# Performance work log

Measured on AMD Instinct MI355X. Metric: run time of the kernel, lower is better.

The kernel has to match this reference:

```python
import jax, jax.numpy as jnp
import numpy as np

N_NODES = 50000
N_EDGES = 800000
F_EXP = 128
F_CNV = 64
HID = 128
N_CLASSES = 10
N_GRAPHS = 64
SLOPE = 0.2


def setup_inputs() -> dict:
    key = jax.random.key(0)
    ks = jax.random.split(key, 24)
    inp = {
        "exp": jax.random.normal(ks[0], (N_NODES, F_EXP), dtype=jnp.float32),
        "cnv": jax.random.normal(ks[1], (N_NODES, F_CNV), dtype=jnp.float32),
        "edge_index": jax.random.randint(ks[2], (2, N_EDGES), 0, N_NODES, dtype=jnp.int64 if jax.config.jax_enable_x64 else jnp.int32),
        "batch": jnp.sort(jax.random.randint(ks[3], (N_NODES,), 0, N_GRAPHS)),
    }
    s = 0.02
    def lin(k, fi, fo):
        kw, kb = jax.random.split(k)
        return (jax.random.normal(kw, (fi, fo), jnp.float32) * s,
                jax.random.normal(kb, (fo,), jnp.float32) * s)
    inp["eps1e"] = jnp.zeros((), jnp.float32)
    inp["W1e"], inp["b1e"] = lin(ks[4], F_EXP, HID)
    inp["eps2e"] = jnp.zeros((), jnp.float32)
    inp["W2e"], inp["b2e"] = lin(ks[5], HID, HID)
    inp["eps1c"] = jnp.zeros((), jnp.float32)
    inp["W1c"], inp["b1c"] = lin(ks[6], F_CNV, HID)
    inp["eps2c"] = jnp.zeros((), jnp.float32)
    inp["W2c"], inp["b2c"] = lin(ks[7], HID, HID)
    inp["Wm"], inp["bm"] = lin(ks[8], 2 * HID, HID)
    inp["Wp1"], inp["bp1"] = lin(ks[9], HID, HID)
    inp["Wp2"], inp["bp2"] = lin(ks[10], HID, N_CLASSES)
    return inp


def _lrelu(x):
    return jnp.where(x > 0, x, SLOPE * x)


def _forward(exp, cnv, src, dst, batch,
             eps1e, W1e, b1e, eps2e, W2e, b2e,
             eps1c, W1c, b1c, eps2c, W2c, b2c,
             Wm, bm, Wp1, bp1, Wp2, bp2):
    N = exp.shape[0]

    def gin(x, eps, W, b):
        # scatter-add neighbor aggregation over edges (self-loops included in src/dst)
        agg = jax.ops.segment_sum(x[src], dst, num_segments=N)
        return ((1.0 + eps) * x + agg) @ W + b

    x_exp = _lrelu(gin(exp, eps1e, W1e, b1e))
    x_exp = _lrelu(gin(x_exp, eps2e, W2e, b2e))
    x_cnv = _lrelu(gin(cnv, eps1c, W1c, b1c))
    x_cnv = _lrelu(gin(x_cnv, eps2c, W2c, b2c))
    x = jnp.concatenate([x_exp, x_cnv], axis=1) @ Wm + bm
    x = _lrelu(x)

    # global mean pool over graph ids
    counts = jax.ops.segment_sum(jnp.ones((N,), x.dtype), batch, num_segments=N_GRAPHS)
    counts = jnp.maximum(counts, 1.0)[:, None]
    graph_repr = jax.ops.segment_sum(x, batch, num_segments=N_GRAPHS) / counts

    logits_nodes = _lrelu(x @ Wp1 + bp1)  # nn.ReLU in mlp -> actually ReLU
    logits_nodes = jnp.maximum(x @ Wp1 + bp1, 0.0) @ Wp2 + bp2
    graph_logits = jax.ops.segment_sum(logits_nodes, batch, num_segments=N_GRAPHS) / counts
    return graph_repr, graph_logits


def reference(exp, cnv, edge_index, batch,
              eps1e, W1e, b1e, eps2e, W2e, b2e,
              eps1c, W1c, b1c, eps2c, W2c, b2c,
              Wm, bm, Wp1, bp1, Wp2, bp2):
    N = exp.shape[0]
    loop = jnp.arange(N, dtype=edge_index.dtype)
    src = jnp.concatenate([edge_index[0], loop])
    dst = jnp.concatenate([edge_index[1], loop])
    return _forward(exp, cnv, src, dst, batch,
                    eps1e, W1e, b1e, eps2e, W2e, b2e,
                    eps1c, W1c, b1c, eps2c, W2c, b2c,
                    Wm, bm, Wp1, bp1, Wp2, bp2)
```

## Files before the change

kernel.cpp:

```cpp
#include <hip/hip_runtime.h>

#define N_NODES 50000
#define N_PAD   50016
#define N_EDGES 800000
#define HID 128
#define NCLS 10
#define NG 64
#define PWAVE 32
#define NB_SCAN ((N_NODES + 255) / 256)

#define EPART 8
#define PRANGE ((N_NODES + EPART - 1) / EPART)
#define ECHUNK 4096
#define NCHUNK ((N_EDGES + ECHUNK - 1) / ECHUNK)

typedef unsigned int uint32;
typedef __attribute__((ext_vector_type(8))) short bf16x8;
typedef __attribute__((ext_vector_type(4))) float f32x4;

__device__ __forceinline__ unsigned short f2bf(float f) {
    uint32 u = __float_as_uint(f);
    uint32 r = u + 0x7fffu + ((u >> 16) & 1u);
    return (unsigned short)(r >> 16);
}
__device__ __forceinline__ float bflo(uint32 v) { return __uint_as_float(v << 16); }
__device__ __forceinline__ float bfhi(uint32 v) { return __uint_as_float(v & 0xffff0000u); }
__device__ __forceinline__ uint32 packbf(float a, float b) {
    return (uint32)f2bf(a) | ((uint32)f2bf(b) << 16);
}


#define PRE_N4E (N_NODES * 128 / 4)
#define PRE_N4C (N_NODES * 64 / 4)
#define PRE_CB ((PRE_N4E + PRE_N4C + 255) / 256)
#define PRE_ZB ((N_NODES + 255) / 256)
#define PRE_TOTAL (PRE_CB + PRE_ZB + 1 + PRE_ZB + 416)

__global__ __launch_bounds__(256) void pre_k(const float* __restrict__ exp_f,
                                             unsigned short* __restrict__ Xe,
                                             const float* __restrict__ cnv_f,
                                             unsigned short* __restrict__ Xc,
                                             int* __restrict__ deg,
                                             float* __restrict__ sums,
                                             const int* __restrict__ batch,
                                             int* __restrict__ gstart,
                                             const float* W1e, const float* W2e,
                                             const float* W1c, const float* W2c,
                                             const float* Wm, const float* Wp1,
                                             unsigned short* WT1e, unsigned short* WT2e,
                                             unsigned short* WT1c, unsigned short* WT2c,
                                             unsigned short* WTm1, unsigned short* WTm2,
                                             unsigned short* WTp1) {
    int b = blockIdx.x;
    int t = threadIdx.x;
    if (b < PRE_CB) {
        int i = b * 256 + t;
        const float* in;
        unsigned short* out;
        if (i < PRE_N4E) { in = exp_f; out = Xe; }
        else { i -= PRE_N4E; if (i >= PRE_N4C) return; in = cnv_f; out = Xc; }
        float4 v = *(const float4*)(in + (size_t)i * 4);
        uint2 o = {packbf(v.x, v.y), packbf(v.z, v.w)};
        *(uint2*)(out + (size_t)i * 4) = o;
        return;
    }
    b -= PRE_CB;
    if (b < PRE_ZB) {
        int i = b * 256 + t;
        if (i < N_NODES) deg[i] = 0;
        return;
    }
    b -= PRE_ZB;
    if (b == 0) {
        for (int i = t; i < 2 * NG * 128; i += 256) sums[i] = 0.f;
        return;
    }
    b -= 1;
    if (b < PRE_ZB) {
        int i = b * 256 + t;
        if (i >= N_NODES) return;
        int bb = batch[i];
        int prev = (i == 0) ? -1 : batch[i - 1];
        for (int g = prev + 1; g <= bb; g++) gstart[g] = i;
        if (i == N_NODES - 1) {
            for (int g = bb + 1; g <= NG; g++) gstart[g] = N_NODES;
        }
        return;
    }
    b -= PRE_ZB;
    const float* W; unsigned short* WT; int i; int K;
    if (b < 64)       { W = W1e; WT = WT1e; i = b * 256 + t;          K = 128; }
    else if (b < 128) { W = W2e; WT = WT2e; i = (b - 64) * 256 + t;   K = 128; }
    else if (b < 160) { W = W1c; WT = WT1c; i = (b - 128) * 256 + t;  K = 64;  }
    else if (b < 224) { W = W2c; WT = WT2c; i = (b - 160) * 256 + t;  K = 128; }
    else if (b < 352) {
        i = (b - 224) * 256 + t;
        int k = i >> 7, n = i & 127;
        unsigned short v = f2bf(Wm[i]);
        if (k < 128) WTm1[n * 128 + k] = v;
        else         WTm2[n * 128 + (k - 128)] = v;
        return;
    }
    else              { W = Wp1; WT = WTp1; i = (b - 352) * 256 + t;  K = 128; }
    int k = i >> 7, n = i & 127;
    if (k < K) WT[n * K + k] = f2bf(W[i]);
}


__global__ __launch_bounds__(256) void count_part_k(const int* __restrict__ dst,
                                                    int* __restrict__ deg) {
    int part = blockIdx.x & 7;
    int chunk = blockIdx.x >> 3;
    int lo = part * PRANGE;
    int hi = min(lo + PRANGE, N_NODES);
    int e0 = chunk * ECHUNK;
    int e1 = min(e0 + ECHUNK, N_EDGES);
    for (int i = e0 + threadIdx.x; i < e1; i += 256) {
        int d = dst[i];
        if (d >= lo && d < hi) atomicAdd(&deg[d], 1);
    }
}

__global__ __launch_bounds__(256) void scatter_part_k(const int* __restrict__ src,
                                                      const int* __restrict__ dst,
                                                      int* __restrict__ cursor,
                                                      int* __restrict__ csr) {
    int part = blockIdx.x & 7;
    int chunk = blockIdx.x >> 3;
    int lo = part * PRANGE;
    int hi = min(lo + PRANGE, N_NODES);
    int e0 = chunk * ECHUNK;
    int e1 = min(e0 + ECHUNK, N_EDGES);
    for (int i = e0 + threadIdx.x; i < e1; i += 256) {
        int d = dst[i];
        if (d >= lo && d < hi) {
            int pos = atomicAdd(&cursor[d], 1);
            csr[pos] = src[i];
        }
    }
}

__device__ __forceinline__ int block_excl_scan_256(int v, int tid, int* total_out) {
    int lane = tid & 63, w = tid >> 6;
    int x = v;
#pragma unroll
    for (int off = 1; off < 64; off <<= 1) {
        int y = __shfl_up(x, off, 64);
        if (lane >= off) x += y;
    }
    __shared__ int wsum[4];
    if (lane == 63) wsum[w] = x;
    __syncthreads();
    int add = 0;
#pragma unroll
    for (int i = 0; i < 4; i++) add += (i < w) ? wsum[i] : 0;
    int total = wsum[0] + wsum[1] + wsum[2] + wsum[3];
    if (total_out) *total_out = total;
    return x - v + add;
}

__global__ __launch_bounds__(256) void scan_partial_k(const int* __restrict__ deg,
                                                      int* __restrict__ rowptr,
                                                      int* __restrict__ blocksum) {
    int tid = threadIdx.x;
    int gid = blockIdx.x * 256 + tid;
    int v = (gid < N_NODES) ? deg[gid] : 0;
    int total;
    int excl = block_excl_scan_256(v, tid, &total);
    if (gid < N_NODES) rowptr[gid] = excl;
    if (tid == 0) blocksum[blockIdx.x] = total;
}

__global__ __launch_bounds__(256) void scan_root_k(const int* __restrict__ blocksum,
                                                   int* __restrict__ blockoff,
                                                   const int* __restrict__ gstart,
                                                   float* __restrict__ invcnt) {
    int tid = threadIdx.x;
    int v = (tid < NB_SCAN) ? blocksum[tid] : 0;
    int excl = block_excl_scan_256(v, tid, nullptr);
    if (tid < NB_SCAN) blockoff[tid] = excl;
    if (tid < NG) {
        int c = gstart[tid + 1] - gstart[tid];
        invcnt[tid] = (c > 0) ? 1.0f / (float)c : 0.0f;
    }
}

__global__ __launch_bounds__(256) void scan_add_k(int* __restrict__ rowptr,
                                                  int* __restrict__ cursor,
                                                  const int* __restrict__ blockoff) {
    int gid = blockIdx.x * 256 + threadIdx.x;
    if (gid < N_NODES) {
        int r = rowptr[gid] + blockoff[blockIdx.x];
        rowptr[gid] = r;
        cursor[gid] = r;
    }
    if (gid == 0) rowptr[N_NODES] = N_EDGES;
}


__device__ __forceinline__ uint32 agg_row128(const uint32* __restrict__ X,
                                             const int* __restrict__ rowptr,
                                             const int* __restrict__ csr,
                                             int n, int lane, float scale) {
    uint32 xv = X[(size_t)n * 64 + lane];
    float a0 = scale * bflo(xv);
    float a1 = scale * bfhi(xv);
    int e = rowptr[n], e1 = rowptr[n + 1];
    for (; e + 16 <= e1; e += 16) {
        int idx[16]; uint32 vv[16];
#pragma unroll
        for (int j = 0; j < 16; j++) idx[j] = csr[e + j];
#pragma unroll
        for (int j = 0; j < 16; j++) vv[j] = X[(size_t)idx[j] * 64 + lane];
#pragma unroll
        for (int j = 0; j < 16; j++) { a0 += bflo(vv[j]); a1 += bfhi(vv[j]); }
    }
    if (e + 8 <= e1) {
        int idx[8]; uint32 vv[8];
#pragma unroll
        for (int j = 0; j < 8; j++) idx[j] = csr[e + j];
#pragma unroll
        for (int j = 0; j < 8; j++) vv[j] = X[(size_t)idx[j] * 64 + lane];
#pragma unroll
        for (int j = 0; j < 8; j++) { a0 += bflo(vv[j]); a1 += bfhi(vv[j]); }
        e += 8;
    }
    if (e + 4 <= e1) {
        int idx[4]; uint32 vv[4];
#pragma unroll
        for (int j = 0; j < 4; j++) idx[j] = csr[e + j];
#pragma unroll
        for (int j = 0; j < 4; j++) vv[j] = X[(size_t)idx[j] * 64 + lane];
#pragma unroll
        for (int j = 0; j < 4; j++) { a0 += bflo(vv[j]); a1 += bfhi(vv[j]); }
        e += 4;
    }
    for (; e < e1; e++) {
        uint32 v = X[(size_t)csr[e] * 64 + lane];
        a0 += bflo(v);
        a1 += bfhi(v);
    }
    return packbf(a0, a1);
}

__device__ __forceinline__ uint32 agg_row64(const uint32* __restrict__ X,
                                            const int* __restrict__ rowptr,
                                            const int* __restrict__ csr,
                                            int n, int lane32, float scale) {
    uint32 xv = X[(size_t)n * 32 + lane32];
    float a0 = scale * bflo(xv);
    float a1 = scale * bfhi(xv);
    int e = rowptr[n], e1 = rowptr[n + 1];
    for (; e + 8 <= e1; e += 8) {
        int idx[8]; uint32 vv[8];
#pragma unroll
        for (int j = 0; j < 8; j++) idx[j] = csr[e + j];
#pragma unroll
        for (int j = 0; j < 8; j++) vv[j] = X[(size_t)idx[j] * 32 + lane32];
#pragma unroll
        for (int j = 0; j < 8; j++) { a0 += bflo(vv[j]); a1 += bfhi(vv[j]); }
    }
    if (e + 4 <= e1) {
        int idx[4]; uint32 vv[4];
#pragma unroll
        for (int j = 0; j < 4; j++) idx[j] = csr[e + j];
#pragma unroll
        for (int j = 0; j < 4; j++) vv[j] = X[(size_t)idx[j] * 32 + lane32];
#pragma unroll
        for (int j = 0; j < 4; j++) { a0 += bflo(vv[j]); a1 += bfhi(vv[j]); }
        e += 4;
    }
    for (; e < e1; e++) {
        uint32 v = X[(size_t)csr[e] * 32 + lane32];
        a0 += bflo(v);
        a1 += bfhi(v);
    }
    return packbf(a0, a1);
}


__global__ __launch_bounds__(256) void agg_gemm_k(const uint32* __restrict__ X1,
                                                  const float* __restrict__ eps1,
                                                  const unsigned short* __restrict__ WT1p,
                                                  const float* __restrict__ b1,
                                                  unsigned short* __restrict__ out1,
                                                  const uint32* __restrict__ X2,
                                                  const float* __restrict__ eps2,
                                                  const unsigned short* __restrict__ WT2p,
                                                  const float* __restrict__ b2,
                                                  unsigned short* __restrict__ out2,
                                                  const int* __restrict__ rowptr,
                                                  const int* __restrict__ csr,
                                                  int nblk1, int K2) {
    __shared__ uint32 lds[32 * 64];
    int blk = blockIdx.x;
    bool second = blk >= nblk1;
    if (second) blk -= nblk1;
    const uint32* X = second ? X2 : X1;
    const float* epsp = second ? eps2 : eps1;
    const unsigned short* WT = second ? WT2p : WT1p;
    const float* bias = second ? b2 : b1;
    unsigned short* out = second ? out2 : out1;
    int K = second ? K2 : 128;

    int tid = threadIdx.x;
    int w = tid >> 6, lane = tid & 63;
    int base = blk * 32;
    float scale = 2.0f + epsp[0];

    if (K == 128) {
        for (int s = 0; s < 8; s++) {
            int lrow = w * 8 + s;
            int n = base + lrow;
            uint32 outv = 0;
            if (n < N_NODES) outv = agg_row128(X, rowptr, csr, n, lane, scale);
            int byte = (lrow * 256 + lane * 4) ^ ((lrow & 7) << 4);
            lds[byte >> 2] = outv;
        }
    } else {
        int half = lane >> 5, lane32 = lane & 31;
        for (int s = 0; s < 4; s++) {
            int lrow = w * 8 + 2 * s + half;
            int n = base + lrow;
            uint32 outv = 0;
            if (n < N_NODES) outv = agg_row64(X, rowptr, csr, n, lane32, scale);
            int byte = (lrow * 128 + lane32 * 4) ^ ((lrow & 7) << 4);
            lds[byte >> 2] = outv;
        }
    }
    __syncthreads();

    int m = lane & 15, g = lane >> 4;
    int lrow = (w & 1) * 16 + m;
    int row16 = base + (w & 1) * 16;
    int col16 = (w >> 1) * 64;

    f32x4 acc[4];
#pragma unroll
    for (int nt = 0; nt < 4; nt++) acc[nt] = (f32x4){0.f, 0.f, 0.f, 0.f};

    const unsigned short* bp = WT + (size_t)(col16 + m) * K + g * 8;
    int rowbytes = K * 2;
    for (int k0 = 0; k0 < K; k0 += 32) {
        int ab = (lrow * rowbytes + (g * 8 + k0) * 2) ^ ((lrow & 7) << 4);
        bf16x8 af = *(const bf16x8*)((const char*)lds + ab);
#pragma unroll
        for (int nt = 0; nt < 4; nt++) {
            bf16x8 bfv = *(const bf16x8*)(bp + (size_t)nt * 16 * K + k0);
            acc[nt] = __builtin_amdgcn_mfma_f32_16x16x32_bf16(af, bfv, acc[nt], 0, 0, 0);
        }
    }

#pragma unroll
    for (int nt = 0; nt < 4; nt++) {
        int col = col16 + nt * 16 + m;
        float bv = bias[col];
#pragma unroll
        for (int r = 0; r < 4; r++) {
            int row = row16 + g * 4 + r;
            if (row < N_NODES) {
                float v = acc[nt][r] + bv;
                v = v > 0.f ? v : 0.2f * v;
                out[(size_t)row * 128 + col] = f2bf(v);
            }
        }
    }
}


__global__ __launch_bounds__(256) void gemm_bf_k(const unsigned short* __restrict__ A1,
                                                 const unsigned short* __restrict__ WT1, int K1,
                                                 const unsigned short* __restrict__ A2,
                                                 const unsigned short* __restrict__ WT2, int K2,
                                                 const float* __restrict__ bias,
                                                 unsigned short* __restrict__ out, int act) {
    int tid = threadIdx.x;
    int w = tid >> 6, l = tid & 63;
    int row16 = blockIdx.x * 32 + (w & 1) * 16;
    int col16 = (w >> 1) * 64;
    int m = l & 15, g = l >> 4;

    f32x4 acc[4];
#pragma unroll
    for (int nt = 0; nt < 4; nt++) acc[nt] = (f32x4){0.f, 0.f, 0.f, 0.f};

    const unsigned short* A = A1;
    const unsigned short* WT = WT1;
    int K = K1;
    for (int pass = 0; pass < 2; ++pass) {
        if (pass) {
            if (A2 == nullptr) break;
            A = A2; WT = WT2; K = K2;
        }
        const unsigned short* ap = A + (size_t)(row16 + m) * K + g * 8;
        const unsigned short* bp = WT + (size_t)(col16 + m) * K + g * 8;
        for (int k0 = 0; k0 < K; k0 += 32) {
            bf16x8 af = *(const bf16x8*)(ap + k0);
#pragma unroll
            for (int nt = 0; nt < 4; nt++) {
                bf16x8 bfv = *(const bf16x8*)(bp + (size_t)nt * 16 * K + k0);
                acc[nt] = __builtin_amdgcn_mfma_f32_16x16x32_bf16(af, bfv, acc[nt], 0, 0, 0);
            }
        }
    }

#pragma unroll
    for (int nt = 0; nt < 4; nt++) {
        int col = col16 + nt * 16 + m;
        float bv = bias[col];
#pragma unroll
        for (int r = 0; r < 4; r++) {
            int row = row16 + g * 4 + r;
            if (row < N_NODES) {
                float v = acc[nt][r] + bv;
                if (act == 1) v = v > 0.f ? v : 0.2f * v;
                else if (act == 2) v = fmaxf(v, 0.f);
                out[(size_t)row * 128 + col] = f2bf(v);
            }
        }
    }
}


__global__ __launch_bounds__(256) void pool2_bf_k(const uint32* __restrict__ D,
                                                  const uint32* __restrict__ T,
                                                  const int* __restrict__ batch,
                                                  float* __restrict__ sumD,
                                                  float* __restrict__ sumT) {
    int wv = (blockIdx.x * 256 + threadIdx.x) >> 6;
    int f = threadIdx.x & 63;
    int i0 = wv * PWAVE;
    if (i0 >= N_NODES) return;
    int i1 = min(i0 + PWAVE, N_NODES);
    float d0 = 0.f, d1 = 0.f, t0 = 0.f, t1 = 0.f;
    int g = batch[i0];
    int i = i0;
    for (; i + 4 <= i1; i += 4) {
        int b0 = batch[i], b1 = batch[i + 1], b2 = batch[i + 2], b3 = batch[i + 3];
        uint32 dv0 = D[(size_t)i * 64 + f];
        uint32 dv1 = D[(size_t)(i + 1) * 64 + f];
        uint32 dv2 = D[(size_t)(i + 2) * 64 + f];
        uint32 dv3 = D[(size_t)(i + 3) * 64 + f];
        uint32 tv0 = T[(size_t)i * 64 + f];
        uint32 tv1 = T[(size_t)(i + 1) * 64 + f];
        uint32 tv2 = T[(size_t)(i + 2) * 64 + f];
        uint32 tv3 = T[(size_t)(i + 3) * 64 + f];
#define POOL_STEP(bg, dv, tv)                                          \
        if (bg != g) {                                                 \
            atomicAdd(&sumD[g * 128 + 2 * f], d0);                     \
            atomicAdd(&sumD[g * 128 + 2 * f + 1], d1);                 \
            atomicAdd(&sumT[g * 128 + 2 * f], t0);                     \
            atomicAdd(&sumT[g * 128 + 2 * f + 1], t1);                 \
            d0 = d1 = t0 = t1 = 0.f; g = bg;                           \
        }                                                              \
        d0 += bflo(dv); d1 += bfhi(dv);                                \
        t0 += bflo(tv); t1 += bfhi(tv);
        POOL_STEP(b0, dv0, tv0)
        POOL_STEP(b1, dv1, tv1)
        POOL_STEP(b2, dv2, tv2)
        POOL_STEP(b3, dv3, tv3)
    }
    for (; i < i1; i++) {
        int bg = batch[i];
        uint32 dv = D[(size_t)i * 64 + f];
        uint32 tv = T[(size_t)i * 64 + f];
        POOL_STEP(bg, dv, tv)
    }
#undef POOL_STEP
    atomicAdd(&sumD[g * 128 + 2 * f], d0);
    atomicAdd(&sumD[g * 128 + 2 * f + 1], d1);
    atomicAdd(&sumT[g * 128 + 2 * f], t0);
    atomicAdd(&sumT[g * 128 + 2 * f + 1], t1);
}


__global__ __launch_bounds__(128) void finalize_k(const float* __restrict__ sumD,
                                                  const float* __restrict__ sumT,
                                                  const float* __restrict__ invcnt,
                                                  const float* __restrict__ Wp2,
                                                  const float* __restrict__ bp2,
                                                  float* __restrict__ out) {
    __shared__ float tr[128];
    int g = blockIdx.x;
    int f = threadIdx.x;
    float ic = invcnt[g];
    out[g * 128 + f] = sumD[g * 128 + f] * ic;
    tr[f] = sumT[g * 128 + f] * ic;
    __syncthreads();
    if (f < NCLS) {
        float acc = (ic > 0.f) ? bp2[f] : 0.f;
        for (int k = 0; k < 128; k++) acc = fmaf(tr[k], Wp2[k * NCLS + f], acc);
        out[NG * 128 + g * NCLS + f] = acc;
    }
}


extern "C" void kernel_launch(void* const* d_in, const int* in_sizes, int n_in,
                              void* d_out, int out_size, void* d_ws, size_t ws_size,
                              hipStream_t stream) {
    const float* exp_f = (const float*)d_in[0];
    const float* cnv_f = (const float*)d_in[1];
    const int*   ei    = (const int*)d_in[2];
    const int*   batch = (const int*)d_in[3];
    const float* eps1e = (const float*)d_in[4];
    const float* W1e   = (const float*)d_in[5];
    const float* b1e   = (const float*)d_in[6];
    const float* eps2e = (const float*)d_in[7];
    const float* W2e   = (const float*)d_in[8];
    const float* b2e   = (const float*)d_in[9];
    const float* eps1c = (const float*)d_in[10];
    const float* W1c   = (const float*)d_in[11];
    const float* b1c   = (const float*)d_in[12];
    const float* eps2c = (const float*)d_in[13];
    const float* W2c   = (const float*)d_in[14];
    const float* b2c   = (const float*)d_in[15];
    const float* Wm    = (const float*)d_in[16];
    const float* bm    = (const float*)d_in[17];
    const float* Wp1   = (const float*)d_in[18];
    const float* bp1   = (const float*)d_in[19];
    const float* Wp2   = (const float*)d_in[20];
    const float* bp2   = (const float*)d_in[21];
    float* out = (float*)d_out;

    char* ws = (char*)d_ws;
    size_t off = 0;
    auto alloc = [&](size_t bytes) -> void* {
        void* p = ws + off;
        off = (off + bytes + 255) & ~(size_t)255;
        return p;
    };
    int* deg      = (int*)alloc((size_t)N_NODES * 4);
    int* rowptr   = (int*)alloc((size_t)(N_NODES + 1) * 4);
    int* cursor   = (int*)alloc((size_t)N_NODES * 4);
    int* csr      = (int*)alloc((size_t)N_EDGES * 4);
    int* gstart   = (int*)alloc((NG + 1) * 4);
    float* invcnt = (float*)alloc(NG * 4);
    int* blocksum = (int*)alloc(NB_SCAN * 4);
    int* blockoff = (int*)alloc(NB_SCAN * 4);
    float* sumD   = (float*)alloc((size_t)NG * 128 * 4);
    float* sumT   = (float*)alloc((size_t)NG * 128 * 4);

    unsigned short* Xe = (unsigned short*)alloc((size_t)N_PAD * 128 * 2);
    unsigned short* Xc = (unsigned short*)alloc((size_t)N_PAD * 64 * 2);
    unsigned short* B  = (unsigned short*)alloc((size_t)N_PAD * 128 * 2);
    unsigned short* C  = (unsigned short*)alloc((size_t)N_PAD * 128 * 2);
    unsigned short* B2 = (unsigned short*)alloc((size_t)N_PAD * 128 * 2);
    unsigned short* C2 = (unsigned short*)alloc((size_t)N_PAD * 128 * 2);
    unsigned short* D  = (unsigned short*)alloc((size_t)N_PAD * 128 * 2);
    unsigned short* T  = (unsigned short*)alloc((size_t)N_PAD * 128 * 2);

    unsigned short* WT1e = (unsigned short*)alloc(128 * 128 * 2);
    unsigned short* WT2e = (unsigned short*)alloc(128 * 128 * 2);
    unsigned short* WT1c = (unsigned short*)alloc(128 * 64 * 2);
    unsigned short* WT2c = (unsigned short*)alloc(128 * 128 * 2);
    unsigned short* WTm1 = (unsigned short*)alloc(128 * 128 * 2);
    unsigned short* WTm2 = (unsigned short*)alloc(128 * 128 * 2);
    unsigned short* WTp1 = (unsigned short*)alloc(128 * 128 * 2);

    const int* src = ei;
    const int* dst = ei + N_EDGES;

    pre_k<<<PRE_TOTAL, 256, 0, stream>>>(exp_f, Xe, cnv_f, Xc, deg, sumD, batch, gstart,
                                         W1e, W2e, W1c, W2c, Wm, Wp1,
                                         WT1e, WT2e, WT1c, WT2c, WTm1, WTm2, WTp1);
    count_part_k<<<NCHUNK * EPART, 256, 0, stream>>>(dst, deg);
    scan_partial_k<<<NB_SCAN, 256, 0, stream>>>(deg, rowptr, blocksum);
    scan_root_k<<<1, 256, 0, stream>>>(blocksum, blockoff, gstart, invcnt);
    scan_add_k<<<NB_SCAN, 256, 0, stream>>>(rowptr, cursor, blockoff);
    scatter_part_k<<<NCHUNK * EPART, 256, 0, stream>>>(src, dst, cursor, csr);

    const int GEMM_GRID = (N_NODES + 31) / 32;

    agg_gemm_k<<<2 * GEMM_GRID, 256, 0, stream>>>((const uint32*)Xe, eps1e, WT1e, b1e, B,
                                                  (const uint32*)Xc, eps1c, WT1c, b1c, C,
                                                  rowptr, csr, GEMM_GRID, 64);
    agg_gemm_k<<<2 * GEMM_GRID, 256, 0, stream>>>((const uint32*)B, eps2e, WT2e, b2e, B2,
                                                  (const uint32*)C, eps2c, WT2c, b2c, C2,
                                                  rowptr, csr, GEMM_GRID, 128);
    gemm_bf_k<<<GEMM_GRID, 256, 0, stream>>>(B2, WTm1, 128, C2, WTm2, 128, bm, D, 1);
    gemm_bf_k<<<GEMM_GRID, 256, 0, stream>>>(D, WTp1, 128, nullptr, nullptr, 0, bp1, T, 2);
    const int POOL_GRID = ((N_NODES + PWAVE - 1) / PWAVE * 64 + 255) / 256;
    pool2_bf_k<<<POOL_GRID, 256, 0, stream>>>((const uint32*)D, (const uint32*)T,
                                              batch, sumD, sumT);
    finalize_k<<<NG, 128, 0, stream>>>(sumD, sumT, invcnt, Wp2, bp2, out);
}
```

Measured before the change: 458.0 us.

## Fuse mix GEMM, head GEMM and mean pooling into one LDS-staged kernel

Replaces the two gemm_bf_k launches and the pool kernel with a single kernel. It computes the mix layer tile, stages it in swizzled shared memory, runs the head GEMM from LDS, and pools both results per block with atomics. This drops the D and T global round trips and two launches, at the cost of more per-block atomics (32-row blocks instead of 32-row waves) and extra syncs. It also shrinks the aggregation inner unroll from 16 to 8 edges, which lowers register pressure but exposes fewer loads in flight.

```diff
diff --git a/kernel.cpp b/kernel.cpp
--- a/kernel.cpp
+++ b/kernel.cpp
@@ -6,7 +6,6 @@
 #define HID 128
 #define NCLS 10
 #define NG 64
-#define PWAVE 32
 #define NB_SCAN ((N_NODES + 255) / 256)
 
 #define EPART 8
@@ -206,16 +205,7 @@
     float a0 = scale * bflo(xv);
     float a1 = scale * bfhi(xv);
     int e = rowptr[n], e1 = rowptr[n + 1];
-    for (; e + 16 <= e1; e += 16) {
-        int idx[16]; uint32 vv[16];
-#pragma unroll
-        for (int j = 0; j < 16; j++) idx[j] = csr[e + j];
-#pragma unroll
-        for (int j = 0; j < 16; j++) vv[j] = X[(size_t)idx[j] * 64 + lane];
-#pragma unroll
-        for (int j = 0; j < 16; j++) { a0 += bflo(vv[j]); a1 += bfhi(vv[j]); }
-    }
-    if (e + 8 <= e1) {
+    for (; e + 8 <= e1; e += 8) {
         int idx[8]; uint32 vv[8];
 #pragma unroll
         for (int j = 0; j < 8; j++) idx[j] = csr[e + j];
@@ -223,7 +213,6 @@
         for (int j = 0; j < 8; j++) vv[j] = X[(size_t)idx[j] * 64 + lane];
 #pragma unroll
         for (int j = 0; j < 8; j++) { a0 += bflo(vv[j]); a1 += bfhi(vv[j]); }
-        e += 8;
     }
     if (e + 4 <= e1) {
         int idx[4]; uint32 vv[4];
@@ -368,109 +357,125 @@
 }
 
 
-__global__ __launch_bounds__(256) void gemm_bf_k(const unsigned short* __restrict__ A1,
-                                                 const unsigned short* __restrict__ WT1, int K1,
-                                                 const unsigned short* __restrict__ A2,
-                                                 const unsigned short* __restrict__ WT2, int K2,
-                                                 const float* __restrict__ bias,
-                                                 unsigned short* __restrict__ out, int act) {
+__global__ __launch_bounds__(256) void mix_head_pool_k(const unsigned short* __restrict__ B2,
+                                                       const unsigned short* __restrict__ WTm1,
+                                                       const unsigned short* __restrict__ C2,
+                                                       const unsigned short* __restrict__ WTm2,
+                                                       const float* __restrict__ bm,
+                                                       const unsigned short* __restrict__ WTp1,
+                                                       const float* __restrict__ bp1,
+                                                       const int* __restrict__ batch,
+                                                       float* __restrict__ sumD,
+                                                       float* __restrict__ sumT,
+                                                       float* __restrict__ outD) {
+    __shared__ uint32 Dl[32 * 64];
+    __shared__ uint32 Tl[32 * 64];
+    __shared__ int bat[32];
     int tid = threadIdx.x;
-    int w = tid >> 6, l = tid & 63;
-    int row16 = blockIdx.x * 32 + (w & 1) * 16;
+    int w = tid >> 6, lane = tid & 63;
+    int base = blockIdx.x * 32;
+    int m = lane & 15, g = lane >> 4;
+    int row16loc = (w & 1) * 16;
+    int row16 = base + row16loc;
     int col16 = (w >> 1) * 64;
-    int m = l & 15, g = l >> 4;
+
+    if (tid < 32) bat[tid] = (base + tid < N_NODES) ? batch[base + tid] : -1;
 
     f32x4 acc[4];
 #pragma unroll
     for (int nt = 0; nt < 4; nt++) acc[nt] = (f32x4){0.f, 0.f, 0.f, 0.f};
-
-    const unsigned short* A = A1;
-    const unsigned short* WT = WT1;
-    int K = K1;
     for (int pass = 0; pass < 2; ++pass) {
-        if (pass) {
-            if (A2 == nullptr) break;
-            A = A2; WT = WT2; K = K2;
-        }
-        const unsigned short* ap = A + (size_t)(row16 + m) * K + g * 8;
-        const unsigned short* bp = WT + (size_t)(col16 + m) * K + g * 8;
-        for (int k0 = 0; k0 < K; k0 += 32) {
+        const unsigned short* A = pass ? C2 : B2;
+        const unsigned short* WT = pass ? WTm2 : WTm1;
+        const unsigned short* ap = A + (size_t)(row16 + m) * 128 + g * 8;
+        const unsigned short* bp = WT + (size_t)(col16 + m) * 128 + g * 8;
+#pragma unroll
+        for (int k0 = 0; k0 < 128; k0 += 32) {
             bf16x8 af = *(const bf16x8*)(ap + k0);
 #pragma unroll
             for (int nt = 0; nt < 4; nt++) {
-                bf16x8 bfv = *(const bf16x8*)(bp + (size_t)nt * 16 * K + k0);
+                bf16x8 bfv = *(const bf16x8*)(bp + (size_t)nt * 16 * 128 + k0);
                 acc[nt] = __builtin_amdgcn_mfma_f32_16x16x32_bf16(af, bfv, acc[nt], 0, 0, 0);
             }
         }
     }
-
 #pragma unroll
     for (int nt = 0; nt < 4; nt++) {
         int col = col16 + nt * 16 + m;
-        float bv = bias[col];
+        float bv = bm[col];
 #pragma unroll
         for (int r = 0; r < 4; r++) {
-            int row = row16 + g * 4 + r;
-            if (row < N_NODES) {
-                float v = acc[nt][r] + bv;
-                if (act == 1) v = v > 0.f ? v : 0.2f * v;
-                else if (act == 2) v = fmaxf(v, 0.f);
-                out[(size_t)row * 128 + col] = f2bf(v);
+            int rl = row16loc + g * 4 + r;
+            float v = acc[nt][r] + bv;
+            v = v > 0.f ? v : 0.2f * v;
+            int byte = (rl * 256 + col * 2) ^ ((rl & 7) << 4);
+            *(unsigned short*)((char*)Dl + byte) = f2bf(v);
+        }
+    }
+    __syncthreads();
+
+    f32x4 acc2[4];
+#pragma unroll
+    for (int nt = 0; nt < 4; nt++) acc2[nt] = (f32x4){0.f, 0.f, 0.f, 0.f};
+    {
+        int lrowA = row16loc + m;
+        const unsigned short* bp = WTp1 + (size_t)(col16 + m) * 128 + g * 8;
+#pragma unroll
+        for (int k0 = 0; k0 < 128; k0 += 32) {
+            int ab = (lrowA * 256 + (g * 8 + k0) * 2) ^ ((lrowA & 7) << 4);
+            bf16x8 af = *(const bf16x8*)((const char*)Dl + ab);
+#pragma unroll
+            for (int nt = 0; nt < 4; nt++) {
+                bf16x8 bfv = *(const bf16x8*)(bp + (size_t)nt * 16 * 128 + k0);
+                acc2[nt] = __builtin_amdgcn_mfma_f32_16x16x32_bf16(af, bfv, acc2[nt], 0, 0, 0);
             }
         }
     }
-}
-
-
-__global__ __launch_bounds__(256) void pool2_bf_k(const uint32* __restrict__ D,
-                                                  const uint32* __restrict__ T,
-                                                  const int* __restrict__ batch,
-                                                  float* __restrict__ sumD,
-                                                  float* __restrict__ sumT) {
-    int wv = (blockIdx.x * 256 + threadIdx.x) >> 6;
-    int f = threadIdx.x & 63;
-    int i0 = wv * PWAVE;
-    if (i0 >= N_NODES) return;
-    int i1 = min(i0 + PWAVE, N_NODES);
-    float d0 = 0.f, d1 = 0.f, t0 = 0.f, t1 = 0.f;
-    int g = batch[i0];
-    int i = i0;
-    for (; i + 4 <= i1; i += 4) {
-        int b0 = batch[i], b1 = batch[i + 1], b2 = batch[i + 2], b3 = batch[i + 3];
-        uint32 dv0 = D[(size_t)i * 64 + f];
-        uint32 dv1 = D[(size_t)(i + 1) * 64 + f];
-        uint32 dv2 = D[(size_t)(i + 2) * 64 + f];
-        uint32 dv3 = D[(size_t)(i + 3) * 64 + f];
-        uint32 tv0 = T[(size_t)i * 64 + f];
-        uint32 tv1 = T[(size_t)(i + 1) * 64 + f];
-        uint32 tv2 = T[(size_t)(i + 2) * 64 + f];
-        uint32 tv3 = T[(size_t)(i + 3) * 64 + f];
-#define POOL_STEP(bg, dv, tv)                                          \
-        if (bg != g) {                                                 \
-            atomicAdd(&sumD[g * 128 + 2 * f], d0);                     \
-            atomicAdd(&sumD[g * 128 + 2 * f + 1], d1);                 \
-            atomicAdd(&sumT[g * 128 + 2 * f], t0);                     \
-            atomicAdd(&sumT[g * 128 + 2 * f + 1], t1);                 \
-            d0 = d1 = t0 = t1 = 0.f; g = bg;                           \
-        }                                                              \
-        d0 += bflo(dv); d1 += bfhi(dv);                                \
-        t0 += bflo(tv); t1 += bfhi(tv);
-        POOL_STEP(b0, dv0, tv0)
-        POOL_STEP(b1, dv1, tv1)
-        POOL_STEP(b2, dv2, tv2)
-        POOL_STEP(b3, dv3, tv3)
-    }
-    for (; i < i1; i++) {
-        int bg = batch[i];
-        uint32 dv = D[(size_t)i * 64 + f];
-        uint32 tv = T[(size_t)i * 64 + f];
-        POOL_STEP(bg, dv, tv)
-    }
-#undef POOL_STEP
-    atomicAdd(&sumD[g * 128 + 2 * f], d0);
-    atomicAdd(&sumD[g * 128 + 2 * f + 1], d1);
-    atomicAdd(&sumT[g * 128 + 2 * f], t0);
-    atomicAdd(&sumT[g * 128 + 2 * f + 1], t1);
+#pragma unroll
+    for (int nt = 0; nt < 4; nt++) {
+        int col = col16 + nt * 16 + m;
+        float bv = bp1[col];
+#pragma unroll
+        for (int r = 0; r < 4; r++) {
+            int rl = row16loc + g * 4 + r;
+            float v = fmaxf(acc2[nt][r] + bv, 0.f);
+            int byte = (rl * 256 + col * 2) ^ ((rl & 7) << 4);
+            *(unsigned short*)((char*)Tl + byte) = f2bf(v);
+        }
+    }
+    __syncthreads();
+
+    if (tid < 128) {
+        int cp = tid & 63;
+        int half = tid >> 6;
+        int r0 = half * 16;
+        int nrow = min(32, N_NODES - base);
+        int rend = min(r0 + 16, nrow);
+        if (r0 < rend) {
+            float d0 = 0.f, d1 = 0.f, t0 = 0.f, t1 = 0.f;
+            int gcur = bat[r0];
+            for (int r = r0; r < rend; r++) {
+                int bg = bat[r];
+                if (bg != gcur) {
+                    atomicAdd(&sumD[gcur * 128 + 2 * cp], d0);
+                    atomicAdd(&sumD[gcur * 128 + 2 * cp + 1], d1);
+                    atomicAdd(&sumT[gcur * 128 + 2 * cp], t0);
+                    atomicAdd(&sumT[gcur * 128 + 2 * cp + 1], t1);
+                    d0 = d1 = t0 = t1 = 0.f; gcur = bg;
+                }
+                int byte = (r * 256 + cp * 4) ^ ((r & 7) << 4);
+                uint32 dv = *(const uint32*)((const char*)Dl + byte);
+                uint32 tv = *(const uint32*)((const char*)Tl + byte);
+                d0 += bflo(dv); d1 += bfhi(dv);
+                t0 += bflo(tv); t1 += bfhi(tv);
+            }
+            atomicAdd(&sumD[gcur * 128 + 2 * cp], d0);
+            atomicAdd(&sumD[gcur * 128 + 2 * cp + 1], d1);
+            atomicAdd(&sumT[gcur * 128 + 2 * cp], t0);
+            atomicAdd(&sumT[gcur * 128 + 2 * cp + 1], t1);
+        }
+    }
+    (void)outD;
 }
 
 
@@ -546,8 +551,6 @@
     unsigned short* C  = (unsigned short*)alloc((size_t)N_PAD * 128 * 2);
     unsigned short* B2 = (unsigned short*)alloc((size_t)N_PAD * 128 * 2);
     unsigned short* C2 = (unsigned short*)alloc((size_t)N_PAD * 128 * 2);
-    unsigned short* D  = (unsigned short*)alloc((size_t)N_PAD * 128 * 2);
-    unsigned short* T  = (unsigned short*)alloc((size_t)N_PAD * 128 * 2);
 
     unsigned short* WT1e = (unsigned short*)alloc(128 * 128 * 2);
     unsigned short* WT2e = (unsigned short*)alloc(128 * 128 * 2);
@@ -577,10 +580,7 @@
     agg_gemm_k<<<2 * GEMM_GRID, 256, 0, stream>>>((const uint32*)B, eps2e, WT2e, b2e, B2,
                                                   (const uint32*)C, eps2c, WT2c, b2c, C2,
                                                   rowptr, csr, GEMM_GRID, 128);
-    gemm_bf_k<<<GEMM_GRID, 256, 0, stream>>>(B2, WTm1, 128, C2, WTm2, 128, bm, D, 1);
-    gemm_bf_k<<<GEMM_GRID, 256, 0, stream>>>(D, WTp1, 128, nullptr, nullptr, 0, bp1, T, 2);
-    const int POOL_GRID = ((N_NODES + PWAVE - 1) / PWAVE * 64 + 255) / 256;
-    pool2_bf_k<<<POOL_GRID, 256, 0, stream>>>((const uint32*)D, (const uint32*)T,
-                                              batch, sumD, sumT);
+    mix_head_pool_k<<<GEMM_GRID, 256, 0, stream>>>(B2, WTm1, C2, WTm2, bm, WTp1, bp1,
+                                                   batch, sumD, sumT, nullptr);
     finalize_k<<<NG, 128, 0, stream>>>(sumD, sumT, invcnt, Wp2, bp2, out);
 }
```

Measured after the change: 426.2 us. 6.9% less time.
